# Optimization experiments

Measured on AMD Instinct MI355X. Metric: run time of the kernel, lower is better.

## Reference

```python
import jax, jax.numpy as jnp
import numpy as np

NUM_HEADS = 8
WIN = 3


def setup_inputs() -> dict:
    key = jax.random.key(0)
    ks = jax.random.split(key, 7)
    C = 64
    b, H, W = 8, 64, 64
    x = jax.random.normal(ks[0], (b, C, H, W), jnp.float32)
    W_qk = jax.random.normal(ks[1], (C, 2 * C), jnp.float32) * 0.05
    b_qk = jax.random.normal(ks[2], (2 * C,), jnp.float32) * 0.05
    W_kv = jax.random.normal(ks[3], (C, 2 * C), jnp.float32) * 0.05
    b_kv = jax.random.normal(ks[4], (2 * C,), jnp.float32) * 0.05
    W_proj = jax.random.normal(ks[5], (C, C), jnp.float32) * 0.05
    b_proj = jax.random.normal(ks[6], (C,), jnp.float32) * 0.05
    return {"x": x, "W_qk": W_qk, "b_qk": b_qk, "W_kv": W_kv, "b_kv": b_kv,
            "W_proj": W_proj, "b_proj": b_proj}


def reference(x, W_qk, b_qk, W_kv, b_kv, W_proj, b_proj):
    b, C, H, W = x.shape
    hd = C // NUM_HEADS
    scale = hd ** -0.5
    B = b * H * W
    L = WIN * WIN

    # Reflection pad (1,1,1,1) then extract all 3x3 windows (stride 1) -> one window per pixel.
    xp = jnp.pad(x, ((0, 0), (0, 0), (1, 1), (1, 1)), mode="reflect")  # (b,C,H+2,W+2)
    patches = jnp.stack(
        [xp[:, :, i:i + H, j:j + W] for i in range(WIN) for j in range(WIN)],
        axis=2,
    )  # (b, C, 9, H, W)
    patches = jnp.transpose(patches, (0, 3, 4, 1, 2))  # (b, H, W, C, 9)
    # Faithful to torch: contiguous (B, C, 3, 3).reshape(B, L, C) scrambles C and L.
    xs = patches.reshape(B, L, C)  # (B, 9, C) -- scrambled layout, as in original

    # pooling_size=1 -> AvgPool2d identity; g_pooling = mean over the 9 tokens
    x_g = jnp.mean(xs, axis=1, keepdims=True)            # (B, 1, C)
    x_f = jnp.concatenate([x_g, xs], axis=1)             # (B, 10, C)
    N = x_f.shape[1]

    # x_raw: per-pixel token, order (b h w) matches window order
    x_raw = jnp.transpose(x, (0, 2, 3, 1)).reshape(B, C)  # (B, C)

    # q / q_ projections
    qk = x_raw @ W_qk + b_qk                              # (B, 2C)
    q = qk[:, :C].reshape(B, NUM_HEADS, hd)               # (B, h, d)
    q_ = qk[:, C:].reshape(B, NUM_HEADS, hd)              # (B, h, d)
    q_value = jnp.sum(q * q_, axis=-1, keepdims=True)     # (B, h, 1)

    # k / v projections over pooled-global + window tokens
    kv = (x_f @ W_kv + b_kv).reshape(B, N, 2, NUM_HEADS, hd)
    k = jnp.transpose(kv[:, :, 0], (0, 2, 1, 3))          # (B, h, N, d)
    v = jnp.transpose(kv[:, :, 1], (0, 2, 1, 3))          # (B, h, N, d)

    logits = jnp.einsum("bhd,bhnd->bhn", q * scale, k)    # (B, h, N)
    logits = jnp.concatenate([logits, q_value], axis=-1)  # (B, h, N+1)
    attn = jax.nn.softmax(logits, axis=-1)

    x_fusion = jnp.einsum("bhn,bhnd->bhd", attn[..., :N], v)  # (B, h, d)
    x_sole = attn[..., N:] * q_                               # (B, h, d)
    out = (x_sole + x_fusion).reshape(B, C)                   # concat heads

    out = out @ W_proj + b_proj                               # (B, C)
    out = out.reshape(b, H, W, C).transpose(0, 3, 1, 2)       # (b, C, H, W)
    return out
```

## Files before the change

kernel.cpp:

```cpp
#include <hip/hip_runtime.h>
#include <math.h>
#include <stdint.h>


#define GS 432
#define RS 72
#define A0 3456
#define B0 5504
#define C0 6528
#define D0 7552

typedef _Float16 h2 __attribute__((ext_vector_type(2)));

static __device__ __forceinline__ h2 h2_of(uint32_t u) {
    return __builtin_bit_cast(h2, u);
}

__global__ __launch_bounds__(256, 2) void pix_attn_main(
    const float* __restrict__ x,
    const float* __restrict__ W_qk,
    const float* __restrict__ b_qk,
    const float* __restrict__ W_kv,
    const float* __restrict__ b_kv,
    const float* __restrict__ W_proj,
    const float* __restrict__ b_proj,
    float* __restrict__ out)
{
    __shared__ uint32_t smem[8576];

    const int tid = threadIdx.x;
    const int j    = blockIdx.x;
    const int g_   = j >> 4;
    const int tile = g_ * 8 + (j & 7);
    const int hg   = (j >> 3) & 1;
    const int bb   = tile >> 6;
    const int t_id = tile & 63;
    const int h0r  = (t_id >> 2) << 2;
    const int w0c  = (t_id & 3) << 4;

    const float* xb = x + (size_t)bb * (64 * 64 * 64);
#pragma unroll
    for (int it = 0; it < 14; ++it) {
        int idx = it * 256 + tid;
        if (idx < 3456) {
            int pair = idx / 108;
            int pix  = idx - pair * 108;
            int r    = pix / 18;
            int cc   = pix - r * 18;
            int gq   = pair >> 2;
            int w    = pair & 3;
            int gr   = h0r + r - 1;
            gr = (gr < 0) ? 1 : ((gr > 63) ? 62 : gr);
            int gc   = w0c + cc - 1;
            gc = (gc < 0) ? 1 : ((gc > 63) ? 62 : gc);
            const float* p0 = xb + ((pair * 2) << 12) + (gr << 6) + gc;
            h2 pk = { (_Float16)p0[0], (_Float16)p0[4096] };
            smem[gq * GS + r * RS + cc * 4 + w] = __builtin_bit_cast(uint32_t, pk);
        }
    }

    h2* wA = (h2*)(smem + A0);
    h2* wB = (h2*)(smem + B0);
    h2* wC = (h2*)(smem + C0);
    h2* wD = (h2*)(smem + D0);
#pragma unroll
    for (int it = 0; it < 8; ++it) {
        int idx = it * 256 + tid;
        int hh = idx >> 9, dd = (idx >> 5) & 15, p = idx & 31;
        int h  = hg * 4 + hh;
        int col = (dd < 8) ? (h * 8 + dd) : (64 + h * 8 + (dd & 7));
        wA[idx] = h2{ (_Float16)W_qk[(2 * p) * 128 + col],
                      (_Float16)W_qk[(2 * p + 1) * 128 + col] };
    }
#pragma unroll
    for (int it = 0; it < 4; ++it) {
        int idx = it * 256 + tid;
        int hh = idx >> 8, c = (idx >> 2) & 63, dp = idx & 3;
        int h  = hg * 4 + hh;
        wB[idx] = h2{ (_Float16)W_kv[c * 128 + h * 8 + 2 * dp],
                      (_Float16)W_kv[c * 128 + h * 8 + 2 * dp + 1] };
    }
#pragma unroll
    for (int it = 0; it < 4; ++it) {
        int idx = it * 256 + tid;
        int hh = idx >> 8, dd = (idx >> 5) & 7, p = idx & 31;
        int h  = hg * 4 + hh;
        int col = 64 + h * 8 + dd;
        wC[idx] = h2{ (_Float16)W_kv[(2 * p) * 128 + col],
                      (_Float16)W_kv[(2 * p + 1) * 128 + col] };
    }
#pragma unroll
    for (int it = 0; it < 4; ++it) {
        int idx = it * 256 + tid;
        int jj = idx >> 4, p = idx & 15;
        wD[idx] = h2{ (_Float16)W_proj[(hg * 32 + 2 * p) * 64 + jj],
                      (_Float16)W_proj[(hg * 32 + 2 * p + 1) * 64 + jj] };
    }
    __syncthreads();

    const int wv   = __builtin_amdgcn_readfirstlane(tid >> 6);
    const int h8   = (hg * 4 + wv) << 3;
    const int lane = tid & 63;
    const int tr   = lane >> 4;
    const int tc   = lane & 15;
    const uint32_t* xl4 = smem + tr * RS + tc * 4;
    const float scale = 0.35355339059327373f;

    float q[8], qp[8];
    {
        h2 a2[16];
        float acc16[16];
#pragma unroll
        for (int dd = 0; dd < 16; ++dd) acc16[dd] = 0.f;
#pragma unroll
        for (int half = 0; half < 2; ++half) {
#pragma unroll
            for (int g = 0; g < 4; ++g) {
                uint4 v = *(const uint4*)(xl4 + (half * 4 + g) * GS + RS + 4);
#pragma unroll
                for (int w = 0; w < 4; ++w)
                    a2[4 * g + w] = h2_of((&v.x)[w]);
            }
#pragma unroll
            for (int dd = 0; dd < 16; ++dd) {
                const uint4* wr4 =
                    (const uint4*)(wA + wv * 512 + dd * 32 + half * 16);
                float acc = acc16[dd];
#pragma unroll
                for (int p4 = 0; p4 < 4; ++p4) {
                    uint4 wv4 = wr4[p4];
#pragma unroll
                    for (int w = 0; w < 4; ++w)
                        acc = __builtin_amdgcn_fdot2(a2[p4 * 4 + w],
                                                     h2_of((&wv4.x)[w]),
                                                     acc, false);
                }
                acc16[dd] = acc;
            }
            __builtin_amdgcn_sched_barrier(0);
        }
#pragma unroll
        for (int dd = 0; dd < 16; ++dd) {
            if (dd < 8) q[dd] = b_qk[h8 + dd] + acc16[dd];
            else        qp[dd & 7] = b_qk[64 + h8 + (dd & 7)] + acc16[dd];
        }
    }
    float qv = 0.f, beta = 0.f;
#pragma unroll
    for (int d = 0; d < 8; ++d) {
        qv   = fmaf(q[d], qp[d], qv);
        beta = fmaf(q[d], b_kv[h8 + d], beta);
    }
    h2 q2[4];
#pragma unroll
    for (int dp = 0; dp < 4; ++dp)
        q2[dp] = h2{ (_Float16)q[2 * dp], (_Float16)q[2 * dp + 1] };
    __builtin_amdgcn_sched_barrier(0);

    h2 u2[64];
    float uf0[9];
#pragma unroll
    for (int c = 0; c < 64; ++c) {
        uint4 wv4 = *(const uint4*)(wB + wv * 256 + c * 4);
        float s = 0.f;
#pragma unroll
        for (int dp = 0; dp < 4; ++dp)
            s = __builtin_amdgcn_fdot2(q2[dp], h2_of((&wv4.x)[dp]), s, false);
        u2[c].x = (_Float16)s;
        if (c < 9) uf0[c] = s;
        else       u2[c - 9].y = (_Float16)s;
        if ((c & 31) == 31) __builtin_amdgcn_sched_barrier(0);
    }
#pragma unroll
    for (int c = 55; c < 64; ++c)
        u2[c].y = (_Float16)uf0[c + 9 - 64];
    __builtin_amdgcn_sched_barrier(0);

    float lg[9];
#pragma unroll
    for (int t = 0; t < 9; ++t) lg[t] = 0.f;
#pragma unroll
    for (int g = 0; g < 8; ++g) {
#pragma unroll
        for (int l = 0; l < 9; ++l) {
            const int wi = l / 3;
            const int wj = l - wi * 3;
            uint4 v = *(const uint4*)(xl4 + g * GS + wi * RS + wj * 4);
#pragma unroll
            for (int w = 0; w < 4; ++w) {
                h2 hv = h2_of((&v.x)[w]);
                const int f0 = 9 * (8 * g + 2 * w) + l;
                const int c0 = f0 & 63;
                const int t0 = f0 >> 6;
                if (c0 < 55) {
                    lg[t0] = __builtin_amdgcn_fdot2(hv, u2[c0], lg[t0], false);
                } else {
                    lg[t0]     = fmaf((float)hv.x, (float)u2[c0].x, lg[t0]);
                    lg[t0 + 1] = fmaf((float)hv.y, (float)u2[c0].y, lg[t0 + 1]);
                }
            }
        }
        if (g & 1) __builtin_amdgcn_sched_barrier(0);
    }

    float pn[9], Pn = 0.f, pqv;
    {
        float lgs = 0.f, l2[11];
#pragma unroll
        for (int t = 0; t < 9; ++t) {
            lgs += lg[t];
            l2[t] = (lg[t] + beta) * scale;
        }
        l2[9]  = (lgs * (1.f / 9.f) + beta) * scale;
        l2[10] = qv;
        float m = l2[0];
#pragma unroll
        for (int i = 1; i < 11; ++i) m = fmaxf(m, l2[i]);
        float pp[11], den = 0.f;
#pragma unroll
        for (int i = 0; i < 11; ++i) { pp[i] = __expf(l2[i] - m); den += pp[i]; }
        float inv = 1.f / den;
#pragma unroll
        for (int t = 0; t < 9; ++t) {
            pn[t] = (pp[t] + pp[9] * (1.f / 9.f)) * inv;
            Pn += pn[t];
        }
        pqv = pp[10] * inv;
    }
    h2 pn2[9], pn2b[8];
#pragma unroll
    for (int t = 0; t < 9; ++t) pn2[t] = h2{ (_Float16)pn[t], (_Float16)pn[t] };
#pragma unroll
    for (int t = 0; t < 8; ++t) pn2b[t] = h2{ (_Float16)pn[t], (_Float16)pn[t + 1] };
    __builtin_amdgcn_sched_barrier(0);

    h2 y2[64];
#pragma unroll
    for (int c = 0; c < 64; ++c) y2[c] = h2{ (_Float16)0.f, (_Float16)0.f };
#pragma unroll
    for (int g = 0; g < 8; ++g) {
#pragma unroll
        for (int l = 0; l < 9; ++l) {
            const int wi = l / 3;
            const int wj = l - wi * 3;
            uint4 v = *(const uint4*)(xl4 + g * GS + wi * RS + wj * 4);
#pragma unroll
            for (int w = 0; w < 4; ++w) {
                h2 a = h2_of((&v.x)[w]);
                const int f0 = 9 * (8 * g + 2 * w) + l;
                const int c0 = f0 & 63;
                const int t0 = f0 >> 6;
                h2 m2 = (c0 < 55) ? pn2[t0] : pn2b[t0];
                y2[c0] = y2[c0] + m2 * a;
            }
        }
        if (g & 1) __builtin_amdgcn_sched_barrier(0);
    }

    h2 y2c[32];
#pragma unroll
    for (int p = 0; p < 32; ++p) {
        float ylo = (float)y2[2 * p].x     + (float)y2[(2 * p + 55) & 63].y;
        float yhi = (float)y2[2 * p + 1].x + (float)y2[(2 * p + 56) & 63].y;
        y2c[p] = h2{ (_Float16)ylo, (_Float16)yhi };
    }
    __builtin_amdgcn_sched_barrier(0);

    float o[8];
#pragma unroll
    for (int dd = 0; dd < 8; ++dd) {
        const uint4* wr4 = (const uint4*)(wC + wv * 256 + dd * 32);
        float acc = fmaf(pqv, qp[dd], Pn * b_kv[64 + h8 + dd]);
#pragma unroll
        for (int p4 = 0; p4 < 8; ++p4) {
            uint4 wv4 = wr4[p4];
#pragma unroll
            for (int w = 0; w < 4; ++w)
                acc = __builtin_amdgcn_fdot2(y2c[p4 * 4 + w],
                                             h2_of((&wv4.x)[w]), acc, false);
        }
        o[dd] = acc;
    }
    __builtin_amdgcn_sched_barrier(0);

    __syncthreads();
    float* pre = (float*)smem;
#pragma unroll
    for (int d = 0; d < 8; ++d)
        pre[lane * 33 + (wv << 3) + d] = o[d];
    __syncthreads();

    const int j0 = wv << 4;
    const float* pl = pre + lane * 33;
    h2 pre2[16];
#pragma unroll
    for (int p = 0; p < 16; ++p)
        pre2[p] = h2{ (_Float16)pl[2 * p], (_Float16)pl[2 * p + 1] };
    float o2[16];
#pragma unroll
    for (int jj = 0; jj < 16; ++jj) {
        const uint4* wr4 = (const uint4*)(wD + (j0 + jj) * 16);
        float acc = (hg == 0) ? b_proj[j0 + jj] : 0.f;
#pragma unroll
        for (int p4 = 0; p4 < 4; ++p4) {
            uint4 wv4 = wr4[p4];
#pragma unroll
            for (int w = 0; w < 4; ++w)
                acc = __builtin_amdgcn_fdot2(pre2[p4 * 4 + w],
                                             h2_of((&wv4.x)[w]), acc, false);
        }
        o2[jj] = acc;
    }
    float* ob = out + (size_t)bb * (64 * 64 * 64);
    const int pr = h0r + tr, pc = w0c + tc;
#pragma unroll
    for (int jj = 0; jj < 16; ++jj)
        unsafeAtomicAdd(&ob[((j0 + jj) << 12) + (pr << 6) + pc], o2[jj]);
}

extern "C" void kernel_launch(void* const* d_in, const int* in_sizes, int n_in,
                              void* d_out, int out_size, void* d_ws, size_t ws_size,
                              hipStream_t stream)
{
    const float* x      = (const float*)d_in[0];
    const float* W_qk   = (const float*)d_in[1];
    const float* b_qk   = (const float*)d_in[2];
    const float* W_kv   = (const float*)d_in[3];
    const float* b_kv   = (const float*)d_in[4];
    const float* W_proj = (const float*)d_in[5];
    const float* b_proj = (const float*)d_in[6];
    float* out = (float*)d_out;

    hipMemsetAsync(out, 0, (size_t)out_size * sizeof(float), stream);
    pix_attn_main<<<1024, 256, 0, stream>>>(x, W_qk, b_qk, W_kv, b_kv,
                                            W_proj, b_proj, out);
}
```

Baseline: 61.21 us.

## Cut register pressure via packed u values and two-pass V aggregation for occupancy 3

Replaces the 64-entry half2 u array with 32 packed words, rebuilding the shifted pairs on the fly with alignbit and mask ops. It also splits the value aggregation into two passes over channel halves, each followed by an immediate dot with a relaid-out V weight (wC2, doubled in size, with paired c and c+9 rows). This drops the y2/y2c register arrays and lets launch bounds rise to 3 blocks per SM. The cost is re-reading x from shared memory in each pass, extra bit-manipulation ALU work, and more LDS per block.

```diff
diff --git a/kernel.cpp b/kernel.cpp
--- a/kernel.cpp
+++ b/kernel.cpp
@@ -7,8 +7,8 @@
 #define RS 72
 #define A0 3456
 #define B0 5504
-#define C0 6528
-#define D0 7552
+#define C0_ 6528
+#define D0 8576
 
 typedef _Float16 h2 __attribute__((ext_vector_type(2)));
 
@@ -16,7 +16,7 @@
     return __builtin_bit_cast(h2, u);
 }
 
-__global__ __launch_bounds__(256, 2) void pix_attn_main(
+__global__ __launch_bounds__(256, 3) void pix_attn_main(
     const float* __restrict__ x,
     const float* __restrict__ W_qk,
     const float* __restrict__ b_qk,
@@ -26,7 +26,7 @@
     const float* __restrict__ b_proj,
     float* __restrict__ out)
 {
-    __shared__ uint32_t smem[8576];
+    __shared__ uint32_t smem[9600];
 
     const int tid = threadIdx.x;
     const int j    = blockIdx.x;
@@ -61,7 +61,7 @@
 
     h2* wA = (h2*)(smem + A0);
     h2* wB = (h2*)(smem + B0);
-    h2* wC = (h2*)(smem + C0);
+    h2* wC2 = (h2*)(smem + C0_);
     h2* wD = (h2*)(smem + D0);
 #pragma unroll
     for (int it = 0; it < 8; ++it) {
@@ -81,13 +81,14 @@
                       (_Float16)W_kv[c * 128 + h * 8 + 2 * dp + 1] };
     }
 #pragma unroll
-    for (int it = 0; it < 4; ++it) {
-        int idx = it * 256 + tid;
-        int hh = idx >> 8, dd = (idx >> 5) & 7, p = idx & 31;
+    for (int it = 0; it < 8; ++it) {
+        int idx = it * 256 + tid;
+        int hh = idx >> 9, rem = idx & 511;
+        int c0 = rem >> 3, dd = rem & 7;
         int h  = hg * 4 + hh;
         int col = 64 + h * 8 + dd;
-        wC[idx] = h2{ (_Float16)W_kv[(2 * p) * 128 + col],
-                      (_Float16)W_kv[(2 * p + 1) * 128 + col] };
+        wC2[idx] = h2{ (_Float16)W_kv[c0 * 128 + col],
+                       (_Float16)W_kv[((c0 + 9) & 63) * 128 + col] };
     }
 #pragma unroll
     for (int it = 0; it < 4; ++it) {
@@ -157,23 +158,20 @@
         q2[dp] = h2{ (_Float16)q[2 * dp], (_Float16)q[2 * dp + 1] };
     __builtin_amdgcn_sched_barrier(0);
 
-    h2 u2[64];
-    float uf0[9];
-#pragma unroll
-    for (int c = 0; c < 64; ++c) {
-        uint4 wv4 = *(const uint4*)(wB + wv * 256 + c * 4);
-        float s = 0.f;
-#pragma unroll
-        for (int dp = 0; dp < 4; ++dp)
-            s = __builtin_amdgcn_fdot2(q2[dp], h2_of((&wv4.x)[dp]), s, false);
-        u2[c].x = (_Float16)s;
-        if (c < 9) uf0[c] = s;
-        else       u2[c - 9].y = (_Float16)s;
-        if ((c & 31) == 31) __builtin_amdgcn_sched_barrier(0);
-    }
-#pragma unroll
-    for (int c = 55; c < 64; ++c)
-        u2[c].y = (_Float16)uf0[c + 9 - 64];
+    uint32_t up[32];
+#pragma unroll
+    for (int p = 0; p < 32; ++p) {
+        uint4 w0 = *(const uint4*)(wB + wv * 256 + (2 * p) * 4);
+        uint4 w1 = *(const uint4*)(wB + wv * 256 + (2 * p + 1) * 4);
+        float s0 = 0.f, s1 = 0.f;
+#pragma unroll
+        for (int dp = 0; dp < 4; ++dp) {
+            s0 = __builtin_amdgcn_fdot2(q2[dp], h2_of((&w0.x)[dp]), s0, false);
+            s1 = __builtin_amdgcn_fdot2(q2[dp], h2_of((&w1.x)[dp]), s1, false);
+        }
+        up[p] = __builtin_bit_cast(uint32_t, h2{ (_Float16)s0, (_Float16)s1 });
+        if ((p & 15) == 15) __builtin_amdgcn_sched_barrier(0);
+    }
     __builtin_amdgcn_sched_barrier(0);
 
     float lg[9];
@@ -193,10 +191,22 @@
                 const int c0 = f0 & 63;
                 const int t0 = f0 >> 6;
                 if (c0 < 55) {
-                    lg[t0] = __builtin_amdgcn_fdot2(hv, u2[c0], lg[t0], false);
+                    uint32_t uu;
+                    if (c0 & 1)
+                        uu = __builtin_amdgcn_alignbit(up[(c0 + 9) >> 1],
+                                                       up[(c0 - 1) >> 1], 16);
+                    else
+                        uu = (up[c0 >> 1] & 0xffffu) |
+                             (up[(c0 + 8) >> 1] & 0xffff0000u);
+                    lg[t0] = __builtin_amdgcn_fdot2(hv, h2_of(uu), lg[t0], false);
                 } else {
-                    lg[t0]     = fmaf((float)hv.x, (float)u2[c0].x, lg[t0]);
-                    lg[t0 + 1] = fmaf((float)hv.y, (float)u2[c0].y, lg[t0 + 1]);
+                    const int c1 = c0 + 9 - 64;
+                    float ux = (c0 & 1) ? (float)h2_of(up[c0 >> 1]).y
+                                        : (float)h2_of(up[c0 >> 1]).x;
+                    float uy = (c1 & 1) ? (float)h2_of(up[c1 >> 1]).y
+                                        : (float)h2_of(up[c1 >> 1]).x;
+                    lg[t0]     = fmaf((float)hv.x, ux, lg[t0]);
+                    lg[t0 + 1] = fmaf((float)hv.y, uy, lg[t0 + 1]);
                 }
             }
         }
@@ -232,56 +242,63 @@
     for (int t = 0; t < 9; ++t) pn2[t] = h2{ (_Float16)pn[t], (_Float16)pn[t] };
 #pragma unroll
     for (int t = 0; t < 8; ++t) pn2b[t] = h2{ (_Float16)pn[t], (_Float16)pn[t + 1] };
+
+    float o[8];
+#pragma unroll
+    for (int d = 0; d < 8; ++d)
+        o[d] = fmaf(pqv, qp[d], Pn * b_kv[64 + h8 + d]);
     __builtin_amdgcn_sched_barrier(0);
 
-    h2 y2[64];
-#pragma unroll
-    for (int c = 0; c < 64; ++c) y2[c] = h2{ (_Float16)0.f, (_Float16)0.f };
-#pragma unroll
-    for (int g = 0; g < 8; ++g) {
-#pragma unroll
-        for (int l = 0; l < 9; ++l) {
-            const int wi = l / 3;
-            const int wj = l - wi * 3;
-            uint4 v = *(const uint4*)(xl4 + g * GS + wi * RS + wj * 4);
-#pragma unroll
-            for (int w = 0; w < 4; ++w) {
-                h2 a = h2_of((&v.x)[w]);
-                const int f0 = 9 * (8 * g + 2 * w) + l;
-                const int c0 = f0 & 63;
-                const int t0 = f0 >> 6;
-                h2 m2 = (c0 < 55) ? pn2[t0] : pn2b[t0];
-                y2[c0] = y2[c0] + m2 * a;
-            }
-        }
-        if (g & 1) __builtin_amdgcn_sched_barrier(0);
-    }
-
-    h2 y2c[32];
-#pragma unroll
-    for (int p = 0; p < 32; ++p) {
-        float ylo = (float)y2[2 * p].x     + (float)y2[(2 * p + 55) & 63].y;
-        float yhi = (float)y2[2 * p + 1].x + (float)y2[(2 * p + 56) & 63].y;
-        y2c[p] = h2{ (_Float16)ylo, (_Float16)yhi };
-    }
-    __builtin_amdgcn_sched_barrier(0);
-
-    float o[8];
-#pragma unroll
-    for (int dd = 0; dd < 8; ++dd) {
-        const uint4* wr4 = (const uint4*)(wC + wv * 256 + dd * 32);
-        float acc = fmaf(pqv, qp[dd], Pn * b_kv[64 + h8 + dd]);
-#pragma unroll
-        for (int p4 = 0; p4 < 8; ++p4) {
-            uint4 wv4 = wr4[p4];
-#pragma unroll
-            for (int w = 0; w < 4; ++w)
-                acc = __builtin_amdgcn_fdot2(y2c[p4 * 4 + w],
-                                             h2_of((&wv4.x)[w]), acc, false);
-        }
-        o[dd] = acc;
-    }
-    __builtin_amdgcn_sched_barrier(0);
+#pragma unroll
+    for (int pass = 0; pass < 2; ++pass) {
+        h2 y2h[32];
+#pragma unroll
+        for (int i = 0; i < 32; ++i) y2h[i] = h2{ (_Float16)0.f, (_Float16)0.f };
+#pragma unroll
+        for (int g = 0; g < 8; ++g) {
+#pragma unroll
+            for (int l = 0; l < 9; ++l) {
+                const int wi = l / 3;
+                const int wj = l - wi * 3;
+                bool any = false;
+#pragma unroll
+                for (int w = 0; w < 4; ++w) {
+                    const int c0w = (9 * (8 * g + 2 * w) + l) & 63;
+                    if ((c0w >> 5) == pass) any = true;
+                }
+                if (any) {
+                    uint4 v = *(const uint4*)(xl4 + g * GS + wi * RS + wj * 4);
+#pragma unroll
+                    for (int w = 0; w < 4; ++w) {
+                        const int f0 = 9 * (8 * g + 2 * w) + l;
+                        const int c0 = f0 & 63;
+                        if ((c0 >> 5) != pass) continue;
+                        const int t0 = f0 >> 6;
+                        h2 a = h2_of((&v.x)[w]);
+                        h2 m2 = (c0 < 55) ? pn2[t0] : pn2b[t0];
+                        y2h[c0 & 31] = y2h[c0 & 31] + m2 * a;
+                    }
+                }
+            }
+            if (g & 1) __builtin_amdgcn_sched_barrier(0);
+        }
+#pragma unroll
+        for (int i = 0; i < 32; ++i) {
+            const int c0 = pass * 32 + i;
+            const uint4* wr4 = (const uint4*)(wC2 + wv * 512 + c0 * 8);
+            uint4 w0 = wr4[0];
+            uint4 w1 = wr4[1];
+#pragma unroll
+            for (int dd = 0; dd < 4; ++dd) {
+                o[dd]     = __builtin_amdgcn_fdot2(y2h[i], h2_of((&w0.x)[dd]),
+                                                   o[dd], false);
+                o[dd + 4] = __builtin_amdgcn_fdot2(y2h[i], h2_of((&w1.x)[dd]),
+                                                   o[dd + 4], false);
+            }
+            if ((i & 15) == 15) __builtin_amdgcn_sched_barrier(0);
+        }
+        __builtin_amdgcn_sched_barrier(0);
+    }
 
     __syncthreads();
     float* pre = (float*)smem;
```

New measurement: 87.52 us. +43.0%, slower.
